# Optimization experiments

Measured on AMD Instinct MI355X. Metric: run time of the kernel, lower is better.

The kernel has to match this reference:

```python
import jax, jax.numpy as jnp
import numpy as np


def setup_inputs() -> dict:
    key = jax.random.key(0)
    k1, _ = jax.random.split(key)
    x = jax.random.normal(k1, (8, 128, 56, 56), dtype=jnp.float32)
    gamma = jnp.array(0.5, dtype=jnp.float32)  # learned scalar (init gamma=0.5)
    return {"x": x, "gamma": gamma}


def reference(x, gamma):
    # conv=False path: query/key/value convs are Identity, so Q=K=V=x flattened.
    B, C, H, W = x.shape
    N = H * W
    v = x.reshape(B, C, N)                          # [B, C, N]
    # energy[b, i, j] = sum_c x[b, c, i] * x[b, c, j]  (Q^T K)
    energy = jnp.einsum('bci,bcj->bij', v, v)       # [B, N, N]
    # multiplicative mask: zero out the diagonal BEFORE softmax (not -inf)
    mask = 1.0 - jnp.eye(N, dtype=energy.dtype)
    attention = jax.nn.softmax(energy * mask, axis=-1)  # [B, N, N]
    # out = bmm(V, attention): out[b, c, j] = sum_i v[b, c, i] * attention[b, i, j]
    out = jnp.einsum('bci,bij->bcj', v, attention)  # [B, C, N]
    out = jax.nn.relu(out).reshape(B, C, H, W)
    y = gamma * out + x
    return (y, out, x, gamma)
```

## Files before the change

### kernel.cpp

```cpp
#include <hip/hip_runtime.h>
#include <math.h>

#define Bb 8
#define Cc 128
#define Nn 3136
#define Np 3200
#define NT 50
#define Mm (Bb*Cc*Nn)
#define PADV 72
#define L2E 1.44269504088896340736f
#define C44 (44.0f * L2E)

#define XT2B (NT*16*64*8)
#define XC2B (NT*8*128*8)

typedef unsigned short u16;
typedef unsigned int   u32;
typedef __attribute__((ext_vector_type(8)))  u16      u16x8;
typedef __attribute__((ext_vector_type(8)))  _Float16 f16x8;
typedef __attribute__((ext_vector_type(4)))  _Float16 f16x4;
typedef __attribute__((ext_vector_type(4)))  float    f32x4;
typedef __attribute__((ext_vector_type(16))) float    f32x16;

__device__ __forceinline__ float exp2fast(float x) {
#if __has_builtin(__builtin_amdgcn_exp2f)
    return __builtin_amdgcn_exp2f(x);
#else
    float r; asm("v_exp_f32 %0, %1" : "=v"(r) : "v"(x)); return r;
#endif
}

__global__ __launch_bounds__(256) void prep_kernel(const float* __restrict__ x,
                                                   const float* __restrict__ gamma_p,
                                                   float* __restrict__ out,
                                                   u16* __restrict__ xt2,
                                                   u16* __restrict__ xc2,
                                                   float* __restrict__ row_d) {
    const int bx = blockIdx.x;
    const int b = bx / 50, nblk = bx % 50;
    const int t = threadIdx.x;

    if (nblk == 49) {
        const u16x8 z8 = {0, 0, 0, 0, 0, 0, 0, 0};
        u16* dt = xt2 + ((size_t)b * NT + 49) * (16 * 64 * 8);
        u16* dc = xc2 + ((size_t)b * NT + 49) * (8 * 128 * 8);
        #pragma unroll
        for (int it = 0; it < 4; ++it) {
            *(u16x8*)&dt[(it * 256 + t) * 8] = z8;
            *(u16x8*)&dc[(it * 256 + t) * 8] = z8;
        }
        if (t < 64) row_d[b * Np + Nn + t] = 1.0f;
        return;
    }

    __shared__ float lx[Cc][65];
    const int n0 = nblk * 64;

    #pragma unroll 8
    for (int r = 0; r < 32; ++r) {
        const int c = r * 4 + (t >> 6);
        const int g = (b * Cc + c) * Nn + n0 + (t & 63);
        lx[c][t & 63] = x[g];
    }
    __syncthreads();

    {
        const int nl = t & 63, cseg = t >> 6;
        u16x8 hv[4];
        #pragma unroll
        for (int cc = 0; cc < 32; ++cc) {
            const _Float16 hh = (_Float16)lx[cseg * 32 + cc][nl];
            hv[cc >> 3][cc & 7] = __builtin_bit_cast(u16, hh);
        }
        u16* base = xt2 + (((size_t)(b * NT + nblk) * 16 + cseg * 4) * 64 + nl) * 8;
        #pragma unroll
        for (int k = 0; k < 4; ++k) *(u16x8*)&base[k * (64 * 8)] = hv[k];
    }
    {
        const int c = t >> 1, half = t & 1;
        u16x8 hv[4];
        #pragma unroll
        for (int k = 0; k < 32; ++k) {
            const _Float16 hh = (_Float16)lx[c][half * 32 + k];
            hv[k >> 3][k & 7] = __builtin_bit_cast(u16, hh);
        }
        u16* base = xc2 + (((size_t)(b * NT + nblk) * 8 + half * 4) * 128 + c) * 8;
        #pragma unroll
        for (int k = 0; k < 4; ++k) *(u16x8*)&base[k * (128 * 8)] = hv[k];
    }
    if (bx == 0 && t == 0) out[(size_t)3 * Mm] = gamma_p[0];
}

__global__ __launch_bounds__(256, 5) void stats_kernel(const u16* __restrict__ xt2,
                                                       float* __restrict__ row_d) {
    const int bx = blockIdx.x;
    const int b = bx & 7, rem = bx >> 3;
    const int i0t = rem >> 3, jq = rem & 7;
    const int t = threadIdx.x;
    const int w = t >> 6, l = t & 63, lane = l & 31, h = l >> 5;
    const int igrp = w & 1, jsub = w >> 1;
    const u16* __restrict__ xb = xt2 + (size_t)b * XT2B;

    f16x8 Bf[8];
    const int irow = igrp * 32 + lane;
    #pragma unroll
    for (int kk = 0; kk < 8; ++kk)
        Bf[kk] = *(const f16x8*)&xb[(((size_t)i0t * 16 + 2 * kk + h) * 64 + irow) * 8];

    const int jt0 = jq * 6 + (jq < 2 ? jq : 2);
    const int jcnt = 6 + (jq < 2 ? 1 : 0);
    const int jrow = jsub * 32 + lane;

    float sa = 0.f, sb = 0.f;
    for (int jt = jt0; jt < jt0 + jcnt; ++jt) {
        const u16* ab = &xb[((size_t)jt * 16 * 64 + jrow) * 8];
        f32x16 ea, eb;
        #pragma unroll
        for (int r = 0; r < 16; ++r) { ea[r] = 0.f; eb[r] = 0.f; }
        __builtin_amdgcn_s_setprio(1);
        #pragma unroll
        for (int kk = 0; kk < 4; ++kk) {
            const f16x8 A0 = *(const f16x8*)&ab[(4 * kk + h) * 512];
            const f16x8 A1 = *(const f16x8*)&ab[(4 * kk + 2 + h) * 512];
            ea = __builtin_amdgcn_mfma_f32_32x32x16_f16(A0, Bf[2 * kk],     ea, 0, 0, 0);
            eb = __builtin_amdgcn_mfma_f32_32x32x16_f16(A1, Bf[2 * kk + 1], eb, 0, 0, 0);
        }
        __builtin_amdgcn_s_setprio(0);

        if (jt == i0t) {
            const bool dsub = (jsub == igrp);
            #pragma unroll
            for (int r = 0; r < 16; ++r) {
                const int mrow = (r & 3) + 8 * (r >> 2) + 4 * h;
                float v = ea[r] + eb[r];
                if (dsub && mrow == lane) v = 0.f;
                const float e = exp2fast(fmaf(v, L2E, -C44));
                if (r & 1) sb += e; else sa += e;
            }
        } else {
            #pragma unroll
            for (int r = 0; r < 16; ++r) {
                const float e = exp2fast(fmaf(ea[r] + eb[r], L2E, -C44));
                if (r & 1) sb += e; else sa += e;
            }
        }
    }
    float ssum = sa + sb;
    ssum += __shfl_xor(ssum, 32, 64);
    if (h == 0) atomicAdd(&row_d[b * Np + i0t * 64 + igrp * 32 + lane], ssum);
}

__global__ __launch_bounds__(256) void conv_kernel(float* __restrict__ row_d) {
    const int i = blockIdx.x * 256 + threadIdx.x;
    row_d[i] = C44 + __log2f(row_d[i]);
}

__global__ __launch_bounds__(256, 4) void out_kernel(const u16* __restrict__ xt2,
                                                     const u16* __restrict__ xc2,
                                                     const float* __restrict__ row_c,
                                                     float* __restrict__ out) {
    __shared__ u16 s_pt[2][64 * PADV];

    const int bx = blockIdx.x;
    const int b = bx & 7, rem = bx >> 3;
    const int j0t = rem / 3, q = rem % 3;
    const int ti0 = q * 17;
    const int ti1 = (q == 2) ? 50 : ti0 + 17;
    const int t = threadIdx.x;
    const int w = t >> 6, l = t & 63, lane = l & 31, h = l >> 5;
    const int isub = w & 1, jgrp = w >> 1;
    const int jg = w & 1,  cp = w >> 1;
    const u16* __restrict__ xtb = xt2 + (size_t)b * XT2B;
    const u16* __restrict__ xcb = xc2 + (size_t)b * XC2B;

    f16x8 Bj[8];
    const int jrow = jgrp * 32 + lane;
    #pragma unroll
    for (int kk = 0; kk < 8; ++kk)
        Bj[kk] = *(const f16x8*)&xtb[(((size_t)j0t * 16 + 2 * kk + h) * 64 + jrow) * 8];

    f32x16 oa, ob;
    #pragma unroll
    for (int r = 0; r < 16; ++r) { oa[r] = 0.f; ob[r] = 0.f; }

    const int arow = isub * 32 + lane;
    const int ptbase = (jgrp * 32 + lane) * PADV + isub * 32;
    const int pbrow = (jg * 32 + lane) * PADV + h * 8;

    for (int ti = ti0; ti < ti1; ++ti) {
        f32x16 ea, eb;
        #pragma unroll
        for (int r = 0; r < 16; ++r) { ea[r] = 0.f; eb[r] = 0.f; }
        const u16* ab = &xtb[((size_t)ti * 16 * 64 + arow) * 8];
        __builtin_amdgcn_s_setprio(1);
        #pragma unroll
        for (int kk = 0; kk < 4; ++kk) {
            const f16x8 A0 = *(const f16x8*)&ab[(4 * kk + h) * 512];
            const f16x8 A1 = *(const f16x8*)&ab[(4 * kk + 2 + h) * 512];
            ea = __builtin_amdgcn_mfma_f32_32x32x16_f16(A0, Bj[2 * kk],     ea, 0, 0, 0);
            eb = __builtin_amdgcn_mfma_f32_32x32x16_f16(A1, Bj[2 * kk + 1], eb, 0, 0, 0);
        }
        __builtin_amdgcn_s_setprio(0);

        u16* pt = &s_pt[ti & 1][0];
        const float* cbase = &row_c[b * Np + ti * 64 + isub * 32];
        if (ti == j0t) {
            const bool dsub = (isub == jgrp);
            #pragma unroll
            for (int qq = 0; qq < 4; ++qq) {
                const f32x4 cv = *(const f32x4*)&cbase[qq * 8 + h * 4];
                f16x4 pv;
                #pragma unroll
                for (int r = 0; r < 4; ++r) {
                    const int m = qq * 8 + h * 4 + r;
                    float v = ea[qq * 4 + r] + eb[qq * 4 + r];
                    if (dsub && m == lane) v = 0.f;
                    pv[r] = (_Float16)exp2fast(fmaf(v, L2E, -cv[r]));
                }
                *(f16x4*)&pt[ptbase + qq * 8 + h * 4] = pv;
            }
        } else {
            #pragma unroll
            for (int qq = 0; qq < 4; ++qq) {
                const f32x4 cv = *(const f32x4*)&cbase[qq * 8 + h * 4];
                f16x4 pv;
                #pragma unroll
                for (int r = 0; r < 4; ++r)
                    pv[r] = (_Float16)exp2fast(
                        fmaf(ea[qq * 4 + r] + eb[qq * 4 + r], L2E, -cv[r]));
                *(f16x4*)&pt[ptbase + qq * 8 + h * 4] = pv;
            }
        }
        __syncthreads();

        const u16* vb = &xcb[((size_t)ti * 8 * 128 + cp * 64 + lane) * 8];
        __builtin_amdgcn_s_setprio(1);
        #pragma unroll
        for (int kk = 0; kk < 4; ++kk) {
            const f16x8 Bp  = *(const f16x8*)&pt[pbrow + kk * 16];
            const f16x8 Av0 = *(const f16x8*)&vb[((2 * kk + h) * 128) * 8];
            const f16x8 Av1 = *(const f16x8*)&vb[((2 * kk + h) * 128 + 32) * 8];
            oa = __builtin_amdgcn_mfma_f32_32x32x16_f16(Av0, Bp, oa, 0, 0, 0);
            ob = __builtin_amdgcn_mfma_f32_32x32x16_f16(Av1, Bp, ob, 0, 0, 0);
        }
        __builtin_amdgcn_s_setprio(0);
    }

    #pragma unroll
    for (int r = 0; r < 16; ++r) {
        const int mrow = (r & 3) + 8 * (r >> 2) + 4 * h;
        const int jj = j0t * 64 + jg * 32 + lane;
        {
            const int c = cp * 64 + mrow;
            const size_t pos = (size_t)(b * Cc + c) * Nn + jj;
            out[(size_t)q * Mm + pos] = oa[r];
        }
        {
            const int c = cp * 64 + 32 + mrow;
            const size_t pos = (size_t)(b * Cc + c) * Nn + jj;
            out[(size_t)q * Mm + pos] = ob[r];
        }
    }
}

__global__ __launch_bounds__(256) void finish_kernel(const float* __restrict__ x,
                                                     const float* __restrict__ gamma_p,
                                                     float* __restrict__ out) {
    const float gamma = gamma_p[0];
    const size_t base = ((size_t)blockIdx.x * 256 + threadIdx.x) * 4;
    const f32x4 pa = *(const f32x4*)&out[base];
    const f32x4 pb = *(const f32x4*)&out[(size_t)Mm + base];
    const f32x4 pc = *(const f32x4*)&out[(size_t)2 * Mm + base];
    const f32x4 xv = *(const f32x4*)&x[base];
    f32x4 yo, oo;
    #pragma unroll
    for (int r = 0; r < 4; ++r) {
        const float o = fmaxf(pa[r] + pb[r] + pc[r], 0.0f);
        oo[r] = o;
        yo[r] = fmaf(gamma, o, xv[r]);
    }
    *(f32x4*)&out[base] = yo;
    *(f32x4*)&out[(size_t)Mm + base] = oo;
    *(f32x4*)&out[(size_t)2 * Mm + base] = xv;
}

extern "C" void kernel_launch(void* const* d_in, const int* in_sizes, int n_in,
                              void* d_out, int out_size, void* d_ws, size_t ws_size,
                              hipStream_t stream) {
    const float* x       = (const float*)d_in[0];
    const float* gamma_p = (const float*)d_in[1];
    float* out = (float*)d_out;

    float* row_d = (float*)d_ws;
    u16* xt2 = (u16*)((char*)d_ws + (1 << 17));
    u16* xc2 = xt2 + (size_t)Bb * XT2B;

    hipMemsetAsync(row_d, 0, (size_t)Bb * Np * sizeof(float), stream);
    prep_kernel  <<<400, 256, 0, stream>>>(x, gamma_p, out, xt2, xc2, row_d);
    stats_kernel <<<3136, 256, 0, stream>>>(xt2, row_d);
    conv_kernel  <<<100, 256, 0, stream>>>(row_d);
    out_kernel   <<<1176, 256, 0, stream>>>(xt2, xc2, row_d, out);
    finish_kernel<<<3136, 256, 0, stream>>>(x, gamma_p, out);
}
```

Baseline: 212.3 us.

## Split out_kernel into two i-halves and software-pipeline A-operand loads

The i-tile range is now split into two halves instead of three, so fewer blocks each process 25 tiles and finish_kernel sums two partials instead of three. Inside the loop, the next tile's A fragments are prefetched into registers while the current energy MFMAs run, the V loads are hoisted before the barrier, and the two energy accumulators are merged into one chain. The goal is to hide global load latency and cut partial-sum traffic. The cost is more register use, so the occupancy bound drops from 4 to 3, and 784 blocks may fill the CUs less evenly.

```diff
diff --git a/kernel.cpp b/kernel.cpp
--- a/kernel.cpp
+++ b/kernel.cpp
@@ -155,7 +155,7 @@
     row_d[i] = C44 + __log2f(row_d[i]);
 }
 
-__global__ __launch_bounds__(256, 4) void out_kernel(const u16* __restrict__ xt2,
+__global__ __launch_bounds__(256, 3) void out_kernel(const u16* __restrict__ xt2,
                                                      const u16* __restrict__ xc2,
                                                      const float* __restrict__ row_c,
                                                      float* __restrict__ out) {
@@ -163,9 +163,8 @@
 
     const int bx = blockIdx.x;
     const int b = bx & 7, rem = bx >> 3;
-    const int j0t = rem / 3, q = rem % 3;
-    const int ti0 = q * 17;
-    const int ti1 = (q == 2) ? 50 : ti0 + 17;
+    const int j0t = rem >> 1, ih = rem & 1;
+    const int ti0 = ih * 25, ti1 = ti0 + 25;
     const int t = threadIdx.x;
     const int w = t >> 6, l = t & 63, lane = l & 31, h = l >> 5;
     const int isub = w & 1, jgrp = w >> 1;
@@ -187,20 +186,28 @@
     const int ptbase = (jgrp * 32 + lane) * PADV + isub * 32;
     const int pbrow = (jg * 32 + lane) * PADV + h * 8;
 
+    f16x8 Ac[8];
+    {
+        const u16* ab = &xtb[((size_t)ti0 * 16 * 64 + arow) * 8];
+        #pragma unroll
+        for (int kk = 0; kk < 8; ++kk)
+            Ac[kk] = *(const f16x8*)&ab[(2 * kk + h) * 512];
+    }
+
     for (int ti = ti0; ti < ti1; ++ti) {
-        f32x16 ea, eb;
-        #pragma unroll
-        for (int r = 0; r < 16; ++r) { ea[r] = 0.f; eb[r] = 0.f; }
-        const u16* ab = &xtb[((size_t)ti * 16 * 64 + arow) * 8];
-        __builtin_amdgcn_s_setprio(1);
-        #pragma unroll
-        for (int kk = 0; kk < 4; ++kk) {
-            const f16x8 A0 = *(const f16x8*)&ab[(4 * kk + h) * 512];
-            const f16x8 A1 = *(const f16x8*)&ab[(4 * kk + 2 + h) * 512];
-            ea = __builtin_amdgcn_mfma_f32_32x32x16_f16(A0, Bj[2 * kk],     ea, 0, 0, 0);
-            eb = __builtin_amdgcn_mfma_f32_32x32x16_f16(A1, Bj[2 * kk + 1], eb, 0, 0, 0);
-        }
-        __builtin_amdgcn_s_setprio(0);
+        const int tn = (ti + 1 < ti1) ? ti + 1 : ti;
+        f16x8 An[8];
+        const u16* abn = &xtb[((size_t)tn * 16 * 64 + arow) * 8];
+        #pragma unroll
+        for (int kk = 0; kk < 8; ++kk)
+            An[kk] = *(const f16x8*)&abn[(2 * kk + h) * 512];
+
+        f32x16 ea;
+        #pragma unroll
+        for (int r = 0; r < 16; ++r) ea[r] = 0.f;
+        #pragma unroll
+        for (int kk = 0; kk < 8; ++kk)
+            ea = __builtin_amdgcn_mfma_f32_32x32x16_f16(Ac[kk], Bj[kk], ea, 0, 0, 0);
 
         u16* pt = &s_pt[ti & 1][0];
         const float* cbase = &row_c[b * Np + ti * 64 + isub * 32];
@@ -213,7 +220,7 @@
                 #pragma unroll
                 for (int r = 0; r < 4; ++r) {
                     const int m = qq * 8 + h * 4 + r;
-                    float v = ea[qq * 4 + r] + eb[qq * 4 + r];
+                    float v = ea[qq * 4 + r];
                     if (dsub && m == lane) v = 0.f;
                     pv[r] = (_Float16)exp2fast(fmaf(v, L2E, -cv[r]));
                 }
@@ -226,24 +233,29 @@
                 f16x4 pv;
                 #pragma unroll
                 for (int r = 0; r < 4; ++r)
-                    pv[r] = (_Float16)exp2fast(
-                        fmaf(ea[qq * 4 + r] + eb[qq * 4 + r], L2E, -cv[r]));
+                    pv[r] = (_Float16)exp2fast(fmaf(ea[qq * 4 + r], L2E, -cv[r]));
                 *(f16x4*)&pt[ptbase + qq * 8 + h * 4] = pv;
             }
         }
+
+        f16x8 Av[4][2];
+        const u16* vb = &xcb[((size_t)ti * 8 * 128 + cp * 64 + lane) * 8];
+        #pragma unroll
+        for (int kk = 0; kk < 4; ++kk) {
+            Av[kk][0] = *(const f16x8*)&vb[((2 * kk + h) * 128) * 8];
+            Av[kk][1] = *(const f16x8*)&vb[((2 * kk + h) * 128 + 32) * 8];
+        }
         __syncthreads();
 
-        const u16* vb = &xcb[((size_t)ti * 8 * 128 + cp * 64 + lane) * 8];
-        __builtin_amdgcn_s_setprio(1);
         #pragma unroll
         for (int kk = 0; kk < 4; ++kk) {
-            const f16x8 Bp  = *(const f16x8*)&pt[pbrow + kk * 16];
-            const f16x8 Av0 = *(const f16x8*)&vb[((2 * kk + h) * 128) * 8];
-            const f16x8 Av1 = *(const f16x8*)&vb[((2 * kk + h) * 128 + 32) * 8];
-            oa = __builtin_amdgcn_mfma_f32_32x32x16_f16(Av0, Bp, oa, 0, 0, 0);
-            ob = __builtin_amdgcn_mfma_f32_32x32x16_f16(Av1, Bp, ob, 0, 0, 0);
-        }
-        __builtin_amdgcn_s_setprio(0);
+            const f16x8 Bp = *(const f16x8*)&pt[pbrow + kk * 16];
+            oa = __builtin_amdgcn_mfma_f32_32x32x16_f16(Av[kk][0], Bp, oa, 0, 0, 0);
+            ob = __builtin_amdgcn_mfma_f32_32x32x16_f16(Av[kk][1], Bp, ob, 0, 0, 0);
+        }
+
+        #pragma unroll
+        for (int kk = 0; kk < 8; ++kk) Ac[kk] = An[kk];
     }
 
     #pragma unroll
@@ -253,12 +265,12 @@
         {
             const int c = cp * 64 + mrow;
             const size_t pos = (size_t)(b * Cc + c) * Nn + jj;
-            out[(size_t)q * Mm + pos] = oa[r];
+            out[(size_t)ih * Mm + pos] = oa[r];
         }
         {
             const int c = cp * 64 + 32 + mrow;
             const size_t pos = (size_t)(b * Cc + c) * Nn + jj;
-            out[(size_t)q * Mm + pos] = ob[r];
+            out[(size_t)ih * Mm + pos] = ob[r];
         }
     }
 }
@@ -270,12 +282,11 @@
     const size_t base = ((size_t)blockIdx.x * 256 + threadIdx.x) * 4;
     const f32x4 pa = *(const f32x4*)&out[base];
     const f32x4 pb = *(const f32x4*)&out[(size_t)Mm + base];
-    const f32x4 pc = *(const f32x4*)&out[(size_t)2 * Mm + base];
     const f32x4 xv = *(const f32x4*)&x[base];
     f32x4 yo, oo;
     #pragma unroll
     for (int r = 0; r < 4; ++r) {
-        const float o = fmaxf(pa[r] + pb[r] + pc[r], 0.0f);
+        const float o = fmaxf(pa[r] + pb[r], 0.0f);
         oo[r] = o;
         yo[r] = fmaf(gamma, o, xv[r]);
     }
@@ -299,6 +310,6 @@
     prep_kernel  <<<400, 256, 0, stream>>>(x, gamma_p, out, xt2, xc2, row_d);
     stats_kernel <<<3136, 256, 0, stream>>>(xt2, row_d);
     conv_kernel  <<<100, 256, 0, stream>>>(row_d);
-    out_kernel   <<<1176, 256, 0, stream>>>(xt2, xc2, row_d, out);
+    out_kernel   <<<784, 256, 0, stream>>>(xt2, xc2, row_d, out);
     finish_kernel<<<3136, 256, 0, stream>>>(x, gamma_p, out);
 }
```

Result: faster. 195.6 us (-7.8%).
